# Kernel optimization log

Hardware: AMD Instinct MI355X
Metric: run time of the kernel (lower is better)

Reference implementation:

```python
import jax, jax.numpy as jnp
import numpy as np

B, S, D = 2, 2048, 1024
H = 16
HD = D // H  # 64


def setup_inputs() -> dict:
    key = jax.random.key(0)
    k1, k2, k3, k4, k5, k6 = jax.random.split(key, 6)
    hidden_states = jax.random.normal(k1, (B, S, D), dtype=jnp.float32)
    attention_mask = jax.random.randint(k2, (B, S), 0, 2, dtype=jnp.int32)
    scale = 1.0 / np.sqrt(D)
    Wq = jax.random.normal(k3, (D, D), dtype=jnp.float32) * scale
    bq = jax.random.normal(k4, (D,), dtype=jnp.float32) * 0.02
    Wk = jax.random.normal(k5, (D, D), dtype=jnp.float32) * scale
    bk = jax.random.normal(k6, (D,), dtype=jnp.float32) * 0.02
    return {"hidden_states": hidden_states, "attention_mask": attention_mask,
            "Wq": Wq, "bq": bq, "Wk": Wk, "bk": bk}


def _split_heads(x):
    # [B, S, D] -> [B, H, S, HD]
    b, s, _ = x.shape
    return x.reshape(b, s, H, HD).transpose(0, 2, 1, 3)


def reference(hidden_states, attention_mask, Wq, bq, Wk, bk):
    dh = jnp.sqrt(jnp.float32(HD))
    q = _split_heads(hidden_states @ Wq + bq)            # [B,H,S,HD]
    k = _split_heads(hidden_states @ Wk + bk)            # [B,H,S,HD]
    v = q + k                                            # value = Q + K
    k_t = -jax.nn.log_sigmoid(-k)                        # negate the logsigmoid(-K) transform
    scores = jnp.einsum('bhqd,bhkd->bhqk', q, k_t) / dh  # [B,H,S,S]
    # mask applied on the QUERY axis (dim 2), broadcast over key axis (faithful to source)
    mask = (attention_mask[:, None, :, None] == 0)       # [B,1,S,1]
    scores = jnp.where(mask, jnp.float32(-10000.0), scores)
    probs = jax.nn.softmax(scores, axis=-1)              # dropout: eval mode (identity)
    ctx = jnp.einsum('bhqk,bhkd->bhqd', probs, v)        # [B,H,S,HD]
    ctx = ctx.transpose(0, 2, 1, 3).reshape(B, S, D)
    return ctx
```

## Files before the change

### kernel.cpp

```cpp
#include <hip/hip_runtime.h>
#include <hip/hip_bf16.h>

#define B_ 2
#define S_ 2048
#define D_ 1024
#define H_ 16
#define HD_ 64

typedef __attribute__((ext_vector_type(8))) short short8;
typedef __attribute__((ext_vector_type(4))) short short4v;
typedef __attribute__((ext_vector_type(4))) float float4v;

typedef const __attribute__((address_space(1))) void* gas_ptr;
typedef __attribute__((address_space(3))) void* las_ptr;

static __device__ inline void gl_lds16(const void* g, void* l) {
  __builtin_amdgcn_global_load_lds((gas_ptr)g, (las_ptr)l, 16, 0, 0);
}

static __device__ inline float b2f(__hip_bfloat16 h) { return __bfloat162float(h); }

static __device__ inline short f2bs(float x) {
  __hip_bfloat16 h = __float2bfloat16(x);
  union { __hip_bfloat16 h; short s; } u; u.h = h; return u.s;
}
static __device__ inline float bs2f(short s) {
  union { short s; __hip_bfloat16 h; } u; u.s = s; return __bfloat162float(u.h);
}
static __device__ inline short4v pk4(float a, float b, float c, float d) {
  union { __hip_bfloat162 h[2]; short4v s; } u;
  u.h[0] = __float22bfloat162_rn(float2{a, b});
  u.h[1] = __float22bfloat162_rn(float2{c, d});
  return u.s;
}

static __device__ inline float4v mfma32(short8 a, short8 b, float4v c) {
  return __builtin_amdgcn_mfma_f32_16x16x32_bf16(a, b, c, 0, 0, 0);
}
static __device__ inline float4v mfma16(short4v a, short4v b, float4v c) {
  return __builtin_amdgcn_mfma_f32_16x16x16bf16_1k(a, b, c, 0, 0, 0);
}

__global__ __launch_bounds__(256) void pre(
    const float* __restrict__ Wq, const float* __restrict__ Wk,
    const float* __restrict__ hs,
    __hip_bfloat16* __restrict__ Wqt, __hip_bfloat16* __restrict__ Wkt,
    __hip_bfloat16* __restrict__ hsb) {
  if (blockIdx.z == 2) {
    const int blk = blockIdx.y * 16 + blockIdx.x;
    for (int it = 0; it < 8; ++it) {
      const size_t i = (size_t)blk * 16384 + it * 2048 + threadIdx.x * 8;
      const float4v v0 = *(const float4v*)(hs + i);
      const float4v v1 = *(const float4v*)(hs + i + 4);
      short8 s;
      for (int j = 0; j < 4; ++j) { s[j] = f2bs(v0[j]); s[4 + j] = f2bs(v1[j]); }
      *(short8*)(hsb + i) = s;
    }
    return;
  }
  const float* W = blockIdx.z ? Wk : Wq;
  __hip_bfloat16* Wt = blockIdx.z ? Wkt : Wqt;
  __shared__ float t[64][65];
  const int n0 = blockIdx.x * 64, k0 = blockIdx.y * 64;
  const int c = threadIdx.x & 63, r0 = threadIdx.x >> 6;
  for (int i = 0; i < 16; ++i) {
    const int r = i * 4 + r0;
    t[c][r] = W[(size_t)(k0 + r) * D_ + n0 + c];
  }
  __syncthreads();
  for (int i = 0; i < 16; ++i) {
    const int rr = i * 4 + r0;
    Wt[(size_t)(n0 + rr) * D_ + k0 + c] = __float2bfloat16(t[rr][c]);
  }
}

__global__ __launch_bounds__(512, 2) void gemm_fused(
    const __hip_bfloat16* __restrict__ A,
    const __hip_bfloat16* __restrict__ Wqt, const __hip_bfloat16* __restrict__ Wkt,
    const float* __restrict__ bq, const float* __restrict__ bk,
    __hip_bfloat16* __restrict__ q_out, __hip_bfloat16* __restrict__ kt_out,
    __hip_bfloat16* __restrict__ vT) {
  const int n0 = blockIdx.x * 128, m0 = blockIdx.y * 128;
  __shared__ __hip_bfloat16 As[2][128 * 32];
  __shared__ __hip_bfloat16 Bq[2][128 * 32];
  __shared__ __hip_bfloat16 Bk[2][128 * 32];
  const int tid = threadIdx.x, wid = tid >> 6, lane = tid & 63;
  const int wm = (wid >> 1) * 32, wn = (wid & 1) * 64;
  const int l15 = lane & 15, l4 = lane >> 4;
  const float4v zz = {0.f, 0.f, 0.f, 0.f};
  float4v accq[2][4], acck[2][4];
  for (int i = 0; i < 2; ++i)
    for (int j = 0; j < 4; ++j) { accq[i][j] = zz; acck[i][j] = zz; }
  const int lrow = wid * 16 + (lane >> 2);
  const int lk8 = (lane & 3) * 8;
  gl_lds16(A + (size_t)(m0 + lrow) * D_ + lk8, As[0] + wid * 512);
  gl_lds16(Wqt + (size_t)(n0 + lrow) * D_ + lk8, Bq[0] + wid * 512);
  gl_lds16(Wkt + (size_t)(n0 + lrow) * D_ + lk8, Bk[0] + wid * 512);
  int p = 0;
  for (int kb = 0; kb < 32; ++kb) {
    __syncthreads();
    if (kb < 31) {
      const int kc = (kb + 1) * 32 + lk8;
      gl_lds16(A + (size_t)(m0 + lrow) * D_ + kc, As[p ^ 1] + wid * 512);
      gl_lds16(Wqt + (size_t)(n0 + lrow) * D_ + kc, Bq[p ^ 1] + wid * 512);
      gl_lds16(Wkt + (size_t)(n0 + lrow) * D_ + kc, Bk[p ^ 1] + wid * 512);
    }
    short8 af[2], bfq[4], bfk[4];
    const int fo = l4 * 8;
    for (int rt = 0; rt < 2; ++rt)
      af[rt] = *(const short8*)(As[p] + (wm + rt * 16 + l15) * 32 + fo);
    for (int ct = 0; ct < 4; ++ct) {
      bfq[ct] = *(const short8*)(Bq[p] + (wn + ct * 16 + l15) * 32 + fo);
      bfk[ct] = *(const short8*)(Bk[p] + (wn + ct * 16 + l15) * 32 + fo);
    }
    for (int rt = 0; rt < 2; ++rt)
      for (int ct = 0; ct < 4; ++ct) {
        accq[rt][ct] = mfma32(af[rt], bfq[ct], accq[rt][ct]);
        acck[rt][ct] = mfma32(af[rt], bfk[ct], acck[rt][ct]);
      }
    p ^= 1;
  }
  float bvq[4], bvk[4];
  for (int ct = 0; ct < 4; ++ct) {
    bvq[ct] = bq[n0 + wn + ct * 16 + l15];
    bvk[ct] = bk[n0 + wn + ct * 16 + l15];
  }
  for (int rt = 0; rt < 2; ++rt)
    for (int ct = 0; ct < 4; ++ct) {
      const int col = n0 + wn + ct * 16 + l15;
      const int h = col >> 6, d = col & 63;
      const int rowb = m0 + wm + rt * 16 + l4 * 4;
      short4v vv;
      for (int r = 0; r < 4; ++r) {
        const int row = rowb + r;
        const float qv = accq[rt][ct][r] + bvq[ct];
        const float kv = acck[rt][ct][r] + bvk[ct];
        const float sp = fmaxf(kv, 0.f) + __logf(1.f + __expf(-fabsf(kv)));
        q_out[(size_t)row * D_ + col] = __float2bfloat16(qv);
        kt_out[(size_t)row * D_ + col] = __float2bfloat16(sp);
        vv[r] = f2bs(qv + kv);
      }
      const int b = rowb >> 11, s = rowb & 2047;
      const int sw = (s & ~63) | (((s >> 4) & 3) << 2) | (((s >> 2) & 3) << 4);
      *(short4v*)(vT + ((size_t)(b * H_ + h) * HD_ + d) * S_ + sw) = vv;
    }
}

__global__ __launch_bounds__(256, 2) void attn(
    const __hip_bfloat16* __restrict__ qb, const __hip_bfloat16* __restrict__ ktb,
    const __hip_bfloat16* __restrict__ vT, const int* __restrict__ mask,
    float* __restrict__ out) {
  __shared__ short smem[32768];
  const int id = blockIdx.x;
  const int xcd = id & 7;
  const int rest = id >> 3;
  const int q0 = (rest & 15) * 128;
  const int hb = (rest >> 4) * 8 + xcd;
  const int h = hb >> 1, b = hb & 1;
  const int tid = threadIdx.x, wid = tid >> 6, lane = tid & 63;
  const int l15 = lane & 15, l4 = lane >> 4;
  const __hip_bfloat16* qh = qb + (size_t)b * S_ * D_ + h * HD_;
  const __hip_bfloat16* kh = ktb + (size_t)b * S_ * D_ + h * HD_;
  const __hip_bfloat16* vh = vT + (size_t)(b * H_ + h) * HD_ * S_;
  const int srow = tid >> 2;
  const int b0 = tid & 3;
  const int sh = srow & 7;
  const int w0 = srow * 64 + ((b0 ^ sh) * 8);
  const int w1 = srow * 64 + (((b0 + 4) ^ sh) * 8);

  const int qlA = wid * 32 + l15, qlB = qlA + 16;
  const int qrA = q0 + qlA, qrB = q0 + qlB;
  const float SC = 0.125f * 1.44269504f;
  const float mqA = (mask[b * S_ + qrA] != 0) ? SC : 0.f;
  const float mqB = (mask[b * S_ + qrB] != 0) ? SC : 0.f;
  const short8 rA0 = *(const short8*)(qh + (size_t)qrA * D_ + l4 * 8);
  const short8 rA1 = *(const short8*)(qh + (size_t)qrA * D_ + 32 + l4 * 8);
  const short8 rB0 = *(const short8*)(qh + (size_t)qrB * D_ + l4 * 8);
  const short8 rB1 = *(const short8*)(qh + (size_t)qrB * D_ + 32 + l4 * 8);
  short8 bqA0, bqA1, bqB0, bqB1;
  for (int j = 0; j < 8; ++j) {
    bqA0[j] = f2bs(bs2f(rA0[j]) * mqA);
    bqA1[j] = f2bs(bs2f(rA1[j]) * mqA);
    bqB0[j] = f2bs(bs2f(rB0[j]) * mqB);
    bqB1[j] = f2bs(bs2f(rB1[j]) * mqB);
  }

  const int lsh = l15 & 7;
  const int ak0off = l15 * 64 + ((l4 ^ lsh) * 8);
  const int ak1off = l15 * 64 + (((l4 + 4) ^ lsh) * 8);
  const int vb0off = ((2 * l4) ^ lsh) * 8;
  const int vb1off = ((2 * l4 + 1) ^ lsh) * 8;

  const float4v zz = {0.f, 0.f, 0.f, 0.f};
  float4v oaccA[4] = {zz, zz, zz, zz};
  float4v oaccB[4] = {zz, zz, zz, zz};
  float lsumA = 0.f, lsumB = 0.f;

  short8 gk0[2], gk1[2], gv0[2], gv1[2];
#pragma unroll
  for (int u = 0; u < 2; ++u) {
    gk0[u] = *(const short8*)(kh + (size_t)(u * 64 + srow) * D_ + b0 * 8);
    gk1[u] = *(const short8*)(kh + (size_t)(u * 64 + srow) * D_ + b0 * 8 + 32);
    gv0[u] = *(const short8*)(vh + (size_t)srow * S_ + u * 64 + b0 * 8);
    gv1[u] = *(const short8*)(vh + (size_t)srow * S_ + u * 64 + b0 * 8 + 32);
  }

  int p = 0;
  for (int c = 0; c < 16; ++c) {
    short* bufp = smem + p * 16384;
#pragma unroll
    for (int u = 0; u < 2; ++u) {
      *(short8*)(bufp + u * 4096 + w0) = gk0[u];
      *(short8*)(bufp + u * 4096 + w1) = gk1[u];
      *(short8*)(bufp + 8192 + u * 4096 + w0) = gv0[u];
      *(short8*)(bufp + 8192 + u * 4096 + w1) = gv1[u];
    }
    __syncthreads();
    if (c < 15) {
      const int kb = (c + 1) * 128;
#pragma unroll
      for (int u = 0; u < 2; ++u) {
        gk0[u] = *(const short8*)(kh + (size_t)(kb + u * 64 + srow) * D_ + b0 * 8);
        gk1[u] = *(const short8*)(kh + (size_t)(kb + u * 64 + srow) * D_ + b0 * 8 + 32);
        gv0[u] = *(const short8*)(vh + (size_t)srow * S_ + kb + u * 64 + b0 * 8);
        gv1[u] = *(const short8*)(vh + (size_t)srow * S_ + kb + u * 64 + b0 * 8 + 32);
      }
    }
#pragma unroll
    for (int u = 0; u < 2; ++u) {
      const short* kbase = bufp + u * 4096;
      const short* vbase = bufp + 8192 + u * 4096;
      short4v pA[4], pB[4];
#pragma unroll
      for (int t = 0; t < 4; ++t) {
        const short8 ak0 = *(const short8*)(kbase + t * 1024 + ak0off);
        const short8 ak1 = *(const short8*)(kbase + t * 1024 + ak1off);
        float4v cA = zz, cB = zz;
        cA = mfma32(ak0, bqA0, cA);
        cA = mfma32(ak1, bqA1, cA);
        cB = mfma32(ak0, bqB0, cB);
        cB = mfma32(ak1, bqB1, cB);
        float eA[4], eB[4];
#pragma unroll
        for (int r = 0; r < 4; ++r) {
          eA[r] = __builtin_amdgcn_exp2f(cA[r]); lsumA += eA[r];
          eB[r] = __builtin_amdgcn_exp2f(cB[r]); lsumB += eB[r];
        }
        pA[t] = pk4(eA[0], eA[1], eA[2], eA[3]);
        pB[t] = pk4(eB[0], eB[1], eB[2], eB[3]);
      }
#pragma unroll
      for (int dt = 0; dt < 4; ++dt) {
        const int rb = (dt * 16 + l15) * 64;
        const short8 av0 = *(const short8*)(vbase + rb + vb0off);
        const short8 av1 = *(const short8*)(vbase + rb + vb1off);
        const short4v a0 = {av0[0], av0[1], av0[2], av0[3]};
        const short4v a1 = {av0[4], av0[5], av0[6], av0[7]};
        const short4v a2 = {av1[0], av1[1], av1[2], av1[3]};
        const short4v a3 = {av1[4], av1[5], av1[6], av1[7]};
        oaccA[dt] = mfma16(a0, pA[0], oaccA[dt]);
        oaccB[dt] = mfma16(a0, pB[0], oaccB[dt]);
        oaccA[dt] = mfma16(a1, pA[1], oaccA[dt]);
        oaccB[dt] = mfma16(a1, pB[1], oaccB[dt]);
        oaccA[dt] = mfma16(a2, pA[2], oaccA[dt]);
        oaccB[dt] = mfma16(a2, pB[2], oaccB[dt]);
        oaccA[dt] = mfma16(a3, pA[3], oaccA[dt]);
        oaccB[dt] = mfma16(a3, pB[3], oaccB[dt]);
      }
    }
    p ^= 1;
  }
  float lA = lsumA + __shfl_xor(lsumA, 16); lA += __shfl_xor(lA, 32);
  float lB = lsumB + __shfl_xor(lsumB, 16); lB += __shfl_xor(lB, 32);
  __syncthreads();
  float* mbuf = (float*)smem;
  float* mlb = (float*)smem + 128 * 68;
#pragma unroll
  for (int dt = 0; dt < 4; ++dt)
#pragma unroll
    for (int r = 0; r < 4; ++r) {
      mbuf[qlA * 68 + dt * 16 + l4 * 4 + r] = oaccA[dt][r];
      mbuf[qlB * 68 + dt * 16 + l4 * 4 + r] = oaccB[dt][r];
    }
  if (l4 == 0) { mlb[qlA] = lA; mlb[qlB] = lB; }
  __syncthreads();
  const int qq = tid >> 1;
  const int dg = (tid & 1) * 32;
  const float li = 1.f / mlb[qq];
  float* orow = out + (size_t)(b * S_ + q0 + qq) * D_ + h * HD_ + dg;
#pragma unroll
  for (int i = 0; i < 8; ++i) {
    float4v v = *(const float4v*)&mbuf[qq * 68 + dg + i * 4];
#pragma unroll
    for (int r = 0; r < 4; ++r) v[r] *= li;
    *(float4v*)(orow + i * 4) = v;
  }
}

extern "C" void kernel_launch(void* const* d_in, const int* in_sizes, int n_in,
                              void* d_out, int out_size, void* d_ws, size_t ws_size,
                              hipStream_t stream) {
  const float* hs = (const float*)d_in[0];
  const int* mask = (const int*)d_in[1];
  const float* Wq = (const float*)d_in[2];
  const float* bq = (const float*)d_in[3];
  const float* Wk = (const float*)d_in[4];
  const float* bk = (const float*)d_in[5];
  float* out = (float*)d_out;
  char* ws = (char*)d_ws;
  const size_t MB = 1u << 20;
  __hip_bfloat16* q_b = (__hip_bfloat16*)(ws + 0 * MB);
  __hip_bfloat16* k_b = (__hip_bfloat16*)(ws + 8 * MB);
  __hip_bfloat16* hsb = (__hip_bfloat16*)(ws + 16 * MB);
  __hip_bfloat16* vT  = (__hip_bfloat16*)(ws + 24 * MB);
  __hip_bfloat16* Wqt = (__hip_bfloat16*)(ws + 32 * MB);
  __hip_bfloat16* Wkt = (__hip_bfloat16*)(ws + 34 * MB);

  pre<<<dim3(16, 16, 3), 256, 0, stream>>>(Wq, Wk, hs, Wqt, Wkt, hsb);
  gemm_fused<<<dim3(8, 32), 512, 0, stream>>>(hsb, Wqt, Wkt, bq, bk, q_b, k_b, vT);
  attn<<<dim3(512), 256, 0, stream>>>(q_b, k_b, vT, mask, out);
}
```

Measured before the change: 164.9 us.

## Load K and V fragments directly from global into registers, dropping LDS staging

The attention kernel no longer stages K and V tiles through shared memory with block-wide barriers. Each wave now loads its own MFMA operand fragments for 64-key chunks straight from global memory into double-buffered registers, prefetching the next chunk while computing the current one. This removes LDS writes and reads and the per-chunk __syncthreads. In exchange, all four waves fetch the same K/V data redundantly from global/L2, register pressure rises, and accesses become narrower and strided rather than coalesced.

```diff
diff --git a/kernel.cpp b/kernel.cpp
--- a/kernel.cpp
+++ b/kernel.cpp
@@ -150,23 +150,17 @@
     const __hip_bfloat16* __restrict__ qb, const __hip_bfloat16* __restrict__ ktb,
     const __hip_bfloat16* __restrict__ vT, const int* __restrict__ mask,
     float* __restrict__ out) {
-  __shared__ short smem[32768];
+  __shared__ float mbuf[128 * 68 + 128];
   const int id = blockIdx.x;
   const int xcd = id & 7;
-  const int rest = id >> 3;
-  const int q0 = (rest & 15) * 128;
-  const int hb = (rest >> 4) * 8 + xcd;
+  const int q0 = ((id >> 3) & 15) * 128;
+  const int hb = (id >> 7) * 8 + xcd;
   const int h = hb >> 1, b = hb & 1;
   const int tid = threadIdx.x, wid = tid >> 6, lane = tid & 63;
   const int l15 = lane & 15, l4 = lane >> 4;
   const __hip_bfloat16* qh = qb + (size_t)b * S_ * D_ + h * HD_;
   const __hip_bfloat16* kh = ktb + (size_t)b * S_ * D_ + h * HD_;
   const __hip_bfloat16* vh = vT + (size_t)(b * H_ + h) * HD_ * S_;
-  const int srow = tid >> 2;
-  const int b0 = tid & 3;
-  const int sh = srow & 7;
-  const int w0 = srow * 64 + ((b0 ^ sh) * 8);
-  const int w1 = srow * 64 + (((b0 + 4) ^ sh) * 8);
 
   const int qlA = wid * 32 + l15, qlB = qlA + 16;
   const int qrA = q0 + qlA, qrB = q0 + qlB;
@@ -185,96 +179,79 @@
     bqB1[j] = f2bs(bs2f(rB1[j]) * mqB);
   }
 
-  const int lsh = l15 & 7;
-  const int ak0off = l15 * 64 + ((l4 ^ lsh) * 8);
-  const int ak1off = l15 * 64 + (((l4 + 4) ^ lsh) * 8);
-  const int vb0off = ((2 * l4) ^ lsh) * 8;
-  const int vb1off = ((2 * l4 + 1) ^ lsh) * 8;
+  const __hip_bfloat16* kp[4];
+#pragma unroll
+  for (int t = 0; t < 4; ++t) kp[t] = kh + (size_t)(t * 16 + l15) * D_ + l4 * 8;
+  const __hip_bfloat16* vp[4];
+#pragma unroll
+  for (int dt = 0; dt < 4; ++dt) vp[dt] = vh + (size_t)(dt * 16 + l15) * S_ + l4 * 16;
 
   const float4v zz = {0.f, 0.f, 0.f, 0.f};
   float4v oaccA[4] = {zz, zz, zz, zz};
   float4v oaccB[4] = {zz, zz, zz, zz};
   float lsumA = 0.f, lsumB = 0.f;
 
-  short8 gk0[2], gk1[2], gv0[2], gv1[2];
-#pragma unroll
-  for (int u = 0; u < 2; ++u) {
-    gk0[u] = *(const short8*)(kh + (size_t)(u * 64 + srow) * D_ + b0 * 8);
-    gk1[u] = *(const short8*)(kh + (size_t)(u * 64 + srow) * D_ + b0 * 8 + 32);
-    gv0[u] = *(const short8*)(vh + (size_t)srow * S_ + u * 64 + b0 * 8);
-    gv1[u] = *(const short8*)(vh + (size_t)srow * S_ + u * 64 + b0 * 8 + 32);
-  }
-
-  int p = 0;
-  for (int c = 0; c < 16; ++c) {
-    short* bufp = smem + p * 16384;
-#pragma unroll
-    for (int u = 0; u < 2; ++u) {
-      *(short8*)(bufp + u * 4096 + w0) = gk0[u];
-      *(short8*)(bufp + u * 4096 + w1) = gk1[u];
-      *(short8*)(bufp + 8192 + u * 4096 + w0) = gv0[u];
-      *(short8*)(bufp + 8192 + u * 4096 + w1) = gv1[u];
-    }
-    __syncthreads();
-    if (c < 15) {
-      const int kb = (c + 1) * 128;
-#pragma unroll
-      for (int u = 0; u < 2; ++u) {
-        gk0[u] = *(const short8*)(kh + (size_t)(kb + u * 64 + srow) * D_ + b0 * 8);
-        gk1[u] = *(const short8*)(kh + (size_t)(kb + u * 64 + srow) * D_ + b0 * 8 + 32);
-        gv0[u] = *(const short8*)(vh + (size_t)srow * S_ + kb + u * 64 + b0 * 8);
-        gv1[u] = *(const short8*)(vh + (size_t)srow * S_ + kb + u * 64 + b0 * 8 + 32);
-      }
-    }
-#pragma unroll
-    for (int u = 0; u < 2; ++u) {
-      const short* kbase = bufp + u * 4096;
-      const short* vbase = bufp + 8192 + u * 4096;
-      short4v pA[4], pB[4];
+  short8 kf[2][8], vf[2][8];
+#pragma unroll
+  for (int t = 0; t < 4; ++t) {
+    kf[0][2 * t] = *(const short8*)(kp[t]);
+    kf[0][2 * t + 1] = *(const short8*)(kp[t] + 32);
+    vf[0][2 * t] = *(const short8*)(vp[t]);
+    vf[0][2 * t + 1] = *(const short8*)(vp[t] + 8);
+  }
+
+  for (int c = 0; c < 32; ++c) {
+    const int s = c & 1, sn = s ^ 1;
+    if (c < 31) {
+      const int kb = (c + 1) * 64;
 #pragma unroll
       for (int t = 0; t < 4; ++t) {
-        const short8 ak0 = *(const short8*)(kbase + t * 1024 + ak0off);
-        const short8 ak1 = *(const short8*)(kbase + t * 1024 + ak1off);
-        float4v cA = zz, cB = zz;
-        cA = mfma32(ak0, bqA0, cA);
-        cA = mfma32(ak1, bqA1, cA);
-        cB = mfma32(ak0, bqB0, cB);
-        cB = mfma32(ak1, bqB1, cB);
-        float eA[4], eB[4];
-#pragma unroll
-        for (int r = 0; r < 4; ++r) {
-          eA[r] = __builtin_amdgcn_exp2f(cA[r]); lsumA += eA[r];
-          eB[r] = __builtin_amdgcn_exp2f(cB[r]); lsumB += eB[r];
-        }
-        pA[t] = pk4(eA[0], eA[1], eA[2], eA[3]);
-        pB[t] = pk4(eB[0], eB[1], eB[2], eB[3]);
-      }
-#pragma unroll
-      for (int dt = 0; dt < 4; ++dt) {
-        const int rb = (dt * 16 + l15) * 64;
-        const short8 av0 = *(const short8*)(vbase + rb + vb0off);
-        const short8 av1 = *(const short8*)(vbase + rb + vb1off);
-        const short4v a0 = {av0[0], av0[1], av0[2], av0[3]};
-        const short4v a1 = {av0[4], av0[5], av0[6], av0[7]};
-        const short4v a2 = {av1[0], av1[1], av1[2], av1[3]};
-        const short4v a3 = {av1[4], av1[5], av1[6], av1[7]};
-        oaccA[dt] = mfma16(a0, pA[0], oaccA[dt]);
-        oaccB[dt] = mfma16(a0, pB[0], oaccB[dt]);
-        oaccA[dt] = mfma16(a1, pA[1], oaccA[dt]);
-        oaccB[dt] = mfma16(a1, pB[1], oaccB[dt]);
-        oaccA[dt] = mfma16(a2, pA[2], oaccA[dt]);
-        oaccB[dt] = mfma16(a2, pB[2], oaccB[dt]);
-        oaccA[dt] = mfma16(a3, pA[3], oaccA[dt]);
-        oaccB[dt] = mfma16(a3, pB[3], oaccB[dt]);
-      }
-    }
-    p ^= 1;
+        kf[sn][2 * t] = *(const short8*)(kp[t] + (size_t)kb * D_);
+        kf[sn][2 * t + 1] = *(const short8*)(kp[t] + (size_t)kb * D_ + 32);
+        vf[sn][2 * t] = *(const short8*)(vp[t] + kb);
+        vf[sn][2 * t + 1] = *(const short8*)(vp[t] + kb + 8);
+      }
+    }
+    short4v pA[4], pB[4];
+#pragma unroll
+    for (int t = 0; t < 4; ++t) {
+      const short8 ak0 = kf[s][2 * t];
+      const short8 ak1 = kf[s][2 * t + 1];
+      float4v cA = zz, cB = zz;
+      cA = mfma32(ak0, bqA0, cA);
+      cA = mfma32(ak1, bqA1, cA);
+      cB = mfma32(ak0, bqB0, cB);
+      cB = mfma32(ak1, bqB1, cB);
+      float eA[4], eB[4];
+#pragma unroll
+      for (int r = 0; r < 4; ++r) {
+        eA[r] = __builtin_amdgcn_exp2f(cA[r]); lsumA += eA[r];
+        eB[r] = __builtin_amdgcn_exp2f(cB[r]); lsumB += eB[r];
+      }
+      pA[t] = pk4(eA[0], eA[1], eA[2], eA[3]);
+      pB[t] = pk4(eB[0], eB[1], eB[2], eB[3]);
+    }
+#pragma unroll
+    for (int dt = 0; dt < 4; ++dt) {
+      const short8 av0 = vf[s][2 * dt];
+      const short8 av1 = vf[s][2 * dt + 1];
+      const short4v a0 = {av0[0], av0[1], av0[2], av0[3]};
+      const short4v a1 = {av0[4], av0[5], av0[6], av0[7]};
+      const short4v a2 = {av1[0], av1[1], av1[2], av1[3]};
+      const short4v a3 = {av1[4], av1[5], av1[6], av1[7]};
+      oaccA[dt] = mfma16(a0, pA[0], oaccA[dt]);
+      oaccB[dt] = mfma16(a0, pB[0], oaccB[dt]);
+      oaccA[dt] = mfma16(a1, pA[1], oaccA[dt]);
+      oaccB[dt] = mfma16(a1, pB[1], oaccB[dt]);
+      oaccA[dt] = mfma16(a2, pA[2], oaccA[dt]);
+      oaccB[dt] = mfma16(a2, pB[2], oaccB[dt]);
+      oaccA[dt] = mfma16(a3, pA[3], oaccA[dt]);
+      oaccB[dt] = mfma16(a3, pB[3], oaccB[dt]);
+    }
   }
   float lA = lsumA + __shfl_xor(lsumA, 16); lA += __shfl_xor(lA, 32);
   float lB = lsumB + __shfl_xor(lsumB, 16); lB += __shfl_xor(lB, 32);
-  __syncthreads();
-  float* mbuf = (float*)smem;
-  float* mlb = (float*)smem + 128 * 68;
+  float* mlb = mbuf + 128 * 68;
 #pragma unroll
   for (int dt = 0; dt < 4; ++dt)
 #pragma unroll
```

Result: slower. 448.8 us (+172.2%).
